# Kernel tuning notes

Measured on AMD Instinct MI355X. Metric: run time of the kernel, lower is better.

Reference implementation:

```python
import jax, jax.numpy as jnp
import numpy as np

N, E, G = 50000, 400000, 64
DIN, HID, H, ED = 128, 32, 8, 5
HC = H * HID            # 256, conv3 out_channels (concat=False, heads=1)
LH, DOUT = 256, 32
NEG_SLOPE = 0.2


def setup_inputs() -> dict:
    key = jax.random.key(0)
    ks = jax.random.split(key, 32)
    rn = lambda k, s, sc=0.05: (jax.random.normal(k, s, jnp.float32) * sc)
    inp = {
        "x": jax.random.normal(ks[0], (N, DIN), jnp.float32),
        "edge_index": jax.random.randint(ks[1], (2, E), 0, N, jnp.int32),
        "edge_attr": jax.random.uniform(ks[2], (E, ED), jnp.float32),
        "batch": jnp.sort(jax.random.randint(ks[3], (N,), 0, G, jnp.int32)),
        # conv1: in=DIN, heads=H, out=HID, concat=True
        "W1": rn(ks[4], (DIN, H * HID)), "as1": rn(ks[5], (H, HID)), "ad1": rn(ks[6], (H, HID)),
        "We1": rn(ks[7], (ED, H * HID)), "ae1": rn(ks[8], (H, HID)), "b1": jnp.zeros((H * HID,), jnp.float32),
        # conv2: in=H*HID, heads=H, out=HID, concat=True
        "W2": rn(ks[9], (H * HID, H * HID)), "as2": rn(ks[10], (H, HID)), "ad2": rn(ks[11], (H, HID)),
        "We2": rn(ks[12], (ED, H * HID)), "ae2": rn(ks[13], (H, HID)), "b2": jnp.zeros((H * HID,), jnp.float32),
        # conv3: in=H*HID, heads=1, out=HC, concat=False
        "W3": rn(ks[14], (H * HID, HC)), "as3": rn(ks[15], (1, HC)), "ad3": rn(ks[16], (1, HC)),
        "We3": rn(ks[17], (ED, HC)), "ae3": rn(ks[18], (1, HC)), "b3": jnp.zeros((HC,), jnp.float32),
        # MLP head
        "fcW1": rn(ks[19], (HC, LH)), "fcb1": jnp.zeros((LH,), jnp.float32),
        "fcW2": rn(ks[20], (LH, DOUT)), "fcb2": jnp.zeros((DOUT,), jnp.float32),
    }
    return inp


def gat_layer(x, src, dst, ea, W, att_s, att_d, We, att_e, bias, heads, out_ch, concat):
    n = x.shape[0]
    h = (x @ W).reshape(n, heads, out_ch)                 # [N,H,C]
    e = (ea @ We).reshape(-1, heads, out_ch)              # [E,H,C]
    a_s = (h * att_s).sum(-1)                             # [N,H]
    a_d = (h * att_d).sum(-1)                             # [N,H]
    a_e = (e * att_e).sum(-1)                             # [E,H]
    alpha = jax.nn.leaky_relu(a_s[src] + a_d[dst] + a_e, NEG_SLOPE)  # [E,H]
    m = jax.ops.segment_max(alpha, dst, num_segments=n)   # segment softmax over dst
    p = jnp.exp(alpha - m[dst])
    denom = jax.ops.segment_sum(p, dst, num_segments=n)
    w = p / (denom[dst] + 1e-16)                          # [E,H]
    msg = h[src] * w[:, :, None]                          # [E,H,C]
    out = jax.ops.segment_sum(msg, dst, num_segments=n)   # [N,H,C]
    out = out.reshape(n, heads * out_ch) if concat else out.mean(axis=1)
    return out + bias


def reference(x, edge_index, edge_attr, batch,
              W1, as1, ad1, We1, ae1, b1,
              W2, as2, ad2, We2, ae2, b2,
              W3, as3, ad3, We3, ae3, b3,
              fcW1, fcb1, fcW2, fcb2):
    src, dst = edge_index[0], edge_index[1]
    h = jax.nn.elu(gat_layer(x, src, dst, edge_attr, W1, as1, ad1, We1, ae1, b1, H, HID, True))
    h = jax.nn.elu(gat_layer(h, src, dst, edge_attr, W2, as2, ad2, We2, ae2, b2, H, HID, True))
    h = jax.nn.elu(gat_layer(h, src, dst, edge_attr, W3, as3, ad3, We3, ae3, b3, 1, HC, False))
    h = jax.nn.gelu(h @ fcW1 + fcb1, approximate=False) @ fcW2 + fcb2   # [N,DOUT]
    # global_mean_pool over batch ids
    sums = jax.ops.segment_sum(h, batch, num_segments=G)
    cnt = jax.ops.segment_sum(jnp.ones((h.shape[0],), h.dtype), batch, num_segments=G)
    return sums / jnp.maximum(cnt, 1.0)[:, None]
```

## Files before the change

### kernel.cpp

```cpp
#include <hip/hip_runtime.h>
#include <math.h>


#define N_NODES 50000
#define N_EDGES 400000
#define N_GRAPH 64
#define DIN     128
#define NHC     256
#define DOUT    32

typedef _Float16 f16x8 __attribute__((ext_vector_type(8)));
typedef _Float16 f16x4 __attribute__((ext_vector_type(4)));
typedef float    f32x4 __attribute__((ext_vector_type(4)));

#define LDP2 72

__device__ __forceinline__ void fma_mix_lo(float& acc, float pj, int w) {
    asm volatile("v_fma_mix_f32 %0, %1, %2, %0 op_sel:[0,0,0] op_sel_hi:[0,1,0]"
                 : "+v"(acc) : "v"(pj), "v"(w));
}
__device__ __forceinline__ void fma_mix_hi(float& acc, float pj, int w) {
    asm volatile("v_fma_mix_f32 %0, %1, %2, %0 op_sel:[0,1,0] op_sel_hi:[0,1,0]"
                 : "+v"(acc) : "v"(pj), "v"(w));
}

__global__ __launch_bounds__(256) void mfma_gemm_kernel(
    const _Float16* __restrict__ Ah, const _Float16* __restrict__ Bh,
    const float* __restrict__ bias, _Float16* __restrict__ Ch,
    const float* __restrict__ asl, const float* __restrict__ adl,
    float* __restrict__ asb, float* __restrict__ adb,
    const int* __restrict__ batch, float* __restrict__ pooled,
    int nrow, int K, int mode)
{
    __shared__ __align__(16) _Float16 sAh[128][LDP2];
    __shared__ __align__(16) _Float16 sBh[64][LDP2];

    const int tid = threadIdx.x, lane = tid & 63, wid = tid >> 6;
    const int wm = wid & 1, wn = wid >> 1;

    int xt, yt;
    if (gridDim.x == 4) {
        int bid = blockIdx.x + (blockIdx.y << 2);
        yt = (bid >> 5) * 8 + (bid & 7);
        xt = (bid >> 3) & 3;
    } else { xt = blockIdx.x; yt = blockIdx.y; }
    const int row0 = yt * 128, col0 = xt * 64;
    if (row0 >= nrow) return;

    const int frow = lane & 15, fk = (lane >> 4) * 8;

    f32x4 acc[4][2] = {};
    f16x8 pA[4], pB[2];

#pragma unroll
    for (int p = 0; p < 4; p++) {
        int idx = tid + p * 256;
        int r = idx >> 3, ch = (idx & 7) * 8;
        int gr = row0 + r;
        pA[p] = (gr < nrow) ? *(const f16x8*)(Ah + (long)gr * K + ch) : (f16x8)0;
    }
#pragma unroll
    for (int p = 0; p < 2; p++) {
        int idx = tid + p * 256;
        int r = idx >> 3, ch = (idx & 7) * 8;
        pB[p] = *(const f16x8*)(Bh + (long)(col0 + r) * K + ch);
    }

    for (int k0 = 0; k0 < K; k0 += 64) {
#pragma unroll
        for (int p = 0; p < 4; p++) {
            int idx = tid + p * 256;
            *(f16x8*)&sAh[idx >> 3][(idx & 7) * 8] = pA[p];
        }
#pragma unroll
        for (int p = 0; p < 2; p++) {
            int idx = tid + p * 256;
            *(f16x8*)&sBh[idx >> 3][(idx & 7) * 8] = pB[p];
        }
        __syncthreads();

        if (k0 + 64 < K) {
            int kn = k0 + 64;
#pragma unroll
            for (int p = 0; p < 4; p++) {
                int idx = tid + p * 256;
                int r = idx >> 3, ch = (idx & 7) * 8;
                int gr = row0 + r;
                pA[p] = (gr < nrow) ? *(const f16x8*)(Ah + (long)gr * K + kn + ch) : (f16x8)0;
            }
#pragma unroll
            for (int p = 0; p < 2; p++) {
                int idx = tid + p * 256;
                int r = idx >> 3, ch = (idx & 7) * 8;
                pB[p] = *(const f16x8*)(Bh + (long)(col0 + r) * K + kn + ch);
            }
        }

#pragma unroll
        for (int sub = 0; sub < 2; sub++) {
            const int fks = fk + sub * 32;
            f16x8 bh[2];
#pragma unroll
            for (int nt = 0; nt < 2; nt++)
                bh[nt] = *(const f16x8*)&sBh[wn * 32 + nt * 16 + frow][fks];
#pragma unroll
            for (int mt = 0; mt < 4; mt++) {
                f16x8 ah = *(const f16x8*)&sAh[wm * 64 + mt * 16 + frow][fks];
#pragma unroll
                for (int nt = 0; nt < 2; nt++)
                    acc[mt][nt] = __builtin_amdgcn_mfma_f32_16x16x32_f16(ah, bh[nt], acc[mt][nt], 0, 0, 0);
            }
        }
        __syncthreads();
    }

    const int crow0 = row0 + wm * 64 + (lane >> 4) * 4;
    const int ccol0 = col0 + wn * 32 + (lane & 15);

    if (mode == 0) {
#pragma unroll
        for (int mt = 0; mt < 4; mt++)
#pragma unroll
            for (int nt = 0; nt < 2; nt++) {
                int col = ccol0 + nt * 16;
#pragma unroll
                for (int r = 0; r < 4; r++) {
                    int row = crow0 + mt * 16 + r;
                    if (row < nrow) Ch[(long)row * 256 + col] = (_Float16)acc[mt][nt][r];
                }
            }
        if (asl != nullptr) {
            const float asl0 = asl[ccol0], asl1 = asl[ccol0 + 16];
            const float adl0 = adl[ccol0], adl1 = adl[ccol0 + 16];
            const int headw = (col0 + wn * 32) >> 5;
#pragma unroll
            for (int mt = 0; mt < 4; mt++) {
#pragma unroll
                for (int r = 0; r < 4; r++) {
                    float s = acc[mt][0][r] * asl0 + acc[mt][1][r] * asl1;
                    float d = acc[mt][0][r] * adl0 + acc[mt][1][r] * adl1;
                    s += __shfl_xor(s, 1); s += __shfl_xor(s, 2);
                    s += __shfl_xor(s, 4); s += __shfl_xor(s, 8);
                    d += __shfl_xor(d, 1); d += __shfl_xor(d, 2);
                    d += __shfl_xor(d, 4); d += __shfl_xor(d, 8);
                    if ((lane & 15) == 0) {
                        int row = crow0 + mt * 16 + r;
                        if (row < nrow) {
                            asb[row * 8 + headw] = s;
                            adb[row * 8 + headw] = d;
                        }
                    }
                }
            }
        }
    } else {
        float* pool = (float*)&sAh[0][0];
        const int g0 = batch[row0];
        const int rlast = (row0 + 127 < nrow) ? row0 + 127 : nrow - 1;
        const int gspan = batch[rlast] - g0 + 1;
        const bool fits = (gspan <= 16);
        for (int i = tid; i < 16 * 64; i += 256) pool[i] = 0.f;
        __syncthreads();

        const float b0 = bias[ccol0], b1 = bias[ccol0 + 16];
        const int lc0 = ccol0 - col0, lc1 = lc0 + 16;
        float sum0 = 0.f, sum1 = 0.f;
        int curg = -1;
#pragma unroll
        for (int mt = 0; mt < 4; mt++) {
#pragma unroll
            for (int r = 0; r < 4; r++) {
                int row = crow0 + mt * 16 + r;
                if (row >= nrow) continue;
                int g = batch[row];
                if (g != curg) {
                    if (curg >= 0) {
                        if (fits) {
                            atomicAdd(&pool[(curg - g0) * 64 + lc0], sum0);
                            atomicAdd(&pool[(curg - g0) * 64 + lc1], sum1);
                        } else {
                            atomicAdd(&pooled[curg * 256 + ccol0], sum0);
                            atomicAdd(&pooled[curg * 256 + ccol0 + 16], sum1);
                        }
                    }
                    curg = g; sum0 = 0.f; sum1 = 0.f;
                }
                float v0 = acc[mt][0][r] + b0;
                float v1 = acc[mt][1][r] + b1;
                sum0 += 0.5f * v0 * (1.f + erff(v0 * 0.7071067811865475f));
                sum1 += 0.5f * v1 * (1.f + erff(v1 * 0.7071067811865475f));
            }
        }
        if (curg >= 0) {
            if (fits) {
                atomicAdd(&pool[(curg - g0) * 64 + lc0], sum0);
                atomicAdd(&pool[(curg - g0) * 64 + lc1], sum1);
            } else {
                atomicAdd(&pooled[curg * 256 + ccol0], sum0);
                atomicAdd(&pooled[curg * 256 + ccol0 + 16], sum1);
            }
        }
        __syncthreads();
        if (fits) {
            for (int i = tid; i < gspan * 64; i += 256) {
                float val = pool[i];
                if (val != 0.f)
                    atomicAdd(&pooled[(g0 + (i >> 6)) * 256 + col0 + (i & 63)], val);
            }
        }
    }
}

#define J0 1600000
#define J1 32768
#define J2 65536
#define J3 65536
#define J4 65536
#define J5 16384
#define J6 N_NODES
#define J7 64
#define JTOT (J0+J1+J2+J3+J4+J5+J6+J7)

__device__ __forceinline__ void t_one(const float* W, _Float16* Bh,
                                      int id, int K, int realN)
{
    int n = id / K, k = id - n * K;
    Bh[id] = (_Float16)W[(long)k * realN + n];
}

__global__ __launch_bounds__(256) void prep_kernel(
    const float* __restrict__ x,
    const float* __restrict__ W1, const float* __restrict__ W2, const float* __restrict__ W3,
    const float* __restrict__ F1,
    _Float16* __restrict__ xh,
    _Float16* __restrict__ W1th, _Float16* __restrict__ W2th,
    _Float16* __restrict__ W3th, _Float16* __restrict__ F1th,
    float* __restrict__ pooled, int* __restrict__ deg, int* __restrict__ gcnt)
{
    int idx = blockIdx.x * 256 + threadIdx.x;
    if (idx < J0) {
        float4 v = ((const float4*)x)[idx];
        f16x4 h;
        h[0] = (_Float16)v.x; h[1] = (_Float16)v.y;
        h[2] = (_Float16)v.z; h[3] = (_Float16)v.w;
        *(f16x4*)(xh + (long)idx * 4) = h;
        return;
    }
    idx -= J0;
    if (idx < J1) { t_one(W1, W1th, idx, DIN, NHC); return; }
    idx -= J1;
    if (idx < J2) { t_one(W2, W2th, idx, NHC, NHC); return; }
    idx -= J2;
    if (idx < J3) { t_one(W3, W3th, idx, NHC, NHC); return; }
    idx -= J3;
    if (idx < J4) { t_one(F1, F1th, idx, NHC, NHC); return; }
    idx -= J4;
    if (idx < J5) { pooled[idx] = 0.f; return; }
    idx -= J5;
    if (idx < J6) { deg[idx] = 0; return; }
    idx -= J6;
    if (idx < J7) { gcnt[idx] = 0; return; }
}

__global__ void me_all_kernel(
    const float* __restrict__ We1, const float* __restrict__ ae1,
    const float* __restrict__ We2, const float* __restrict__ ae2,
    const float* __restrict__ We3, const float* __restrict__ ae3,
    float* __restrict__ MeAll)
{
    int l = blockIdx.x;
    const float* We = (l == 0) ? We1 : (l == 1) ? We2 : We3;
    const float* ae = (l == 0) ? ae1 : (l == 1) ? ae2 : ae3;
    int H = (l == 2) ? 1 : 8, C = (l == 2) ? 256 : 32;
    int t = threadIdx.x;
    if (t >= 5 * H) return;
    int j = t / H, hh = t - j * H;
    float s = 0.f;
    for (int c = 0; c < C; c++) s += We[j * NHC + hh * C + c] * ae[hh * C + c];
    MeAll[l * 40 + j * H + hh] = s;
}

__global__ __launch_bounds__(256) void asd_kernel(
    const _Float16* __restrict__ h, const float* __restrict__ atts, const float* __restrict__ attd,
    float* __restrict__ asb, float* __restrict__ adb, int total)
{
    int n = blockIdx.x * 256 + threadIdx.x;
    if (n >= total) return;
    const f16x8* hp = (const f16x8*)(h + (long)n * NHC);
    const float4* sp = (const float4*)atts;
    const float4* dp = (const float4*)attd;
    float ss = 0.f, dd = 0.f;
    for (int c = 0; c < NHC / 8; c++) {
        f16x8 hv = hp[c];
        float4 s1 = sp[2 * c], s2 = sp[2 * c + 1];
        float4 d1 = dp[2 * c], d2 = dp[2 * c + 1];
        ss += (float)hv[0] * s1.x + (float)hv[1] * s1.y + (float)hv[2] * s1.z + (float)hv[3] * s1.w
            + (float)hv[4] * s2.x + (float)hv[5] * s2.y + (float)hv[6] * s2.z + (float)hv[7] * s2.w;
        dd += (float)hv[0] * d1.x + (float)hv[1] * d1.y + (float)hv[2] * d1.z + (float)hv[3] * d1.w
            + (float)hv[4] * d2.x + (float)hv[5] * d2.y + (float)hv[6] * d2.z + (float)hv[7] * d2.w;
    }
    asb[n * 8] = ss; adb[n * 8] = dd;
}

__global__ __launch_bounds__(256) void count_hist_kernel(
    const int* __restrict__ ei, const int* __restrict__ batch,
    int* __restrict__ deg, int* __restrict__ gcnt, int E, int N)
{
    __shared__ int hist[N_GRAPH];
    int t = threadIdx.x;
    if (t < N_GRAPH) hist[t] = 0;
    __syncthreads();
    int i = blockIdx.x * 256 + t;
    if (i < E) atomicAdd(&deg[ei[E + i]], 1);
    if (i < N) atomicAdd(&hist[batch[i]], 1);
    __syncthreads();
    if (t < N_GRAPH && hist[t] > 0) atomicAdd(&gcnt[t], hist[t]);
}

__global__ __launch_bounds__(256) void scan_block_kernel(
    const int* __restrict__ deg, int* __restrict__ rowstart, int* __restrict__ partial, int n)
{
    __shared__ int s[256];
    int i = blockIdx.x * 256 + threadIdx.x;
    int v = (i < n) ? deg[i] : 0;
    s[threadIdx.x] = v;
    __syncthreads();
    for (int off = 1; off < 256; off <<= 1) {
        int t = (threadIdx.x >= off) ? s[threadIdx.x - off] : 0;
        __syncthreads();
        s[threadIdx.x] += t;
        __syncthreads();
    }
    if (i < n) rowstart[i] = s[threadIdx.x] - v;
    if (threadIdx.x == 255) partial[blockIdx.x] = s[255];
}

__global__ __launch_bounds__(256) void scan_partial_kernel(int* __restrict__ partial, int nb)
{
    __shared__ int s[256];
    int v = (threadIdx.x < nb) ? partial[threadIdx.x] : 0;
    s[threadIdx.x] = v;
    __syncthreads();
    for (int off = 1; off < 256; off <<= 1) {
        int t = (threadIdx.x >= off) ? s[threadIdx.x - off] : 0;
        __syncthreads();
        s[threadIdx.x] += t;
        __syncthreads();
    }
    if (threadIdx.x < nb) partial[threadIdx.x] = s[threadIdx.x] - v;
}

__global__ __launch_bounds__(256) void scan_add_kernel(
    int* __restrict__ rowstart, const int* __restrict__ partial, int* __restrict__ cursor,
    int n, int E)
{
    int i = blockIdx.x * 256 + threadIdx.x;
    if (i < n) {
        int v = rowstart[i] + partial[blockIdx.x];
        rowstart[i] = v;
        cursor[i] = v;
    }
    if (i == 0) rowstart[n] = E;
}

__global__ __launch_bounds__(256) void fill_kernel(
    const int* __restrict__ ei, int* __restrict__ cursor, int2* __restrict__ csr2, int E)
{
    int e = blockIdx.x * 256 + threadIdx.x;
    if (e >= E) return;
    int dst = ei[E + e];
    int pos = atomicAdd(&cursor[dst], 1);
    csr2[pos] = make_int2(ei[e], e);
}

__global__ __launch_bounds__(256) void aec_kernel(
    const int2* __restrict__ csr2, const float* __restrict__ ea,
    const float* __restrict__ MeAll,
    int* __restrict__ csr, _Float16* __restrict__ aec, int E)
{
    int pos = blockIdx.x * 256 + threadIdx.x;
    if (pos >= E) return;
    int2 se = csr2[pos];
    csr[pos] = se.x;
    const float* eap = ea + (long)se.y * 5;
    float e0 = eap[0], e1 = eap[1], e2 = eap[2], e3 = eap[3], e4 = eap[4];
#pragma unroll
    for (int l = 0; l < 2; l++) {
        const float* Me = MeAll + l * 40;
        f16x8 v;
#pragma unroll
        for (int hh = 0; hh < 8; hh++) {
            float s = e0 * Me[hh] + e1 * Me[8 + hh] + e2 * Me[16 + hh]
                    + e3 * Me[24 + hh] + e4 * Me[32 + hh];
            v[hh] = (_Float16)s;
        }
        *(f16x8*)(aec + (long)l * N_EDGES * 8 + (long)pos * 8) = v;
    }
    const float* Me2 = MeAll + 80;
    float s2 = e0 * Me2[0] + e1 * Me2[1] + e2 * Me2[2] + e3 * Me2[3] + e4 * Me2[4];
    f16x8 v2;
#pragma unroll
    for (int hh = 0; hh < 8; hh++) v2[hh] = (_Float16)s2;
    *(f16x8*)(aec + (long)2 * N_EDGES * 8 + (long)pos * 8) = v2;
}

__global__ __launch_bounds__(256) void gat_agg_kernel(
    const int* __restrict__ rowstart, const int* __restrict__ csr,
    const _Float16* __restrict__ aec, const float* __restrict__ asb,
    const float* __restrict__ adb,
    const _Float16* __restrict__ h, const float* __restrict__ bias,
    _Float16* __restrict__ Oh, int H, int clog2)
{
    int node = blockIdx.x * 4 + (threadIdx.x >> 6);
    if (node >= N_NODES) return;
    const int lane = threadIdx.x & 63;
    const int half = lane >> 5;
    const int c8   = (lane & 31) * 8;
    const int hc   = c8 >> clog2;
    const int heff = lane & (H - 1);
    const int grp  = lane >> 3;

    const float adn = adb[node * 8 + heff];
    const int beg = rowstart[node], end = rowstart[node + 1];

    float acc[8] = {};
    float den = 0.f;

    for (int i = beg; i < end; i += 8) {
        int idx = i + grp;
        const bool valid = (idx < end);
        if (!valid) idx = end - 1;
        const int sj = csr[idx];
        const float ae = (float)aec[(long)idx * 8 + heff];
        float al = asb[sj * 8 + heff] + adn + ae;
        al = fmaxf(al, 0.2f * al);
        const float pv = valid ? __expf(al) : 0.f;
#pragma unroll
        for (int jj = 0; jj < 4; jj++) {
            const int j = jj * 2 + half;
            const float pj = __shfl(pv, j * 8 + hc);
            const int srcj = __shfl(sj, j * 8);
            const int4 hw = *(const int4*)(h + (long)srcj * NHC + c8);
            den += pj;
            fma_mix_lo(acc[0], pj, hw.x); fma_mix_hi(acc[1], pj, hw.x);
            fma_mix_lo(acc[2], pj, hw.y); fma_mix_hi(acc[3], pj, hw.y);
            fma_mix_lo(acc[4], pj, hw.z); fma_mix_hi(acc[5], pj, hw.z);
            fma_mix_lo(acc[6], pj, hw.w); fma_mix_hi(acc[7], pj, hw.w);
        }
    }

    den += __shfl_xor(den, 32);
#pragma unroll
    for (int k = 0; k < 8; k++)
        acc[k] += __shfl_xor(acc[k], 32);

    if (half == 0) {
        const float w = 1.0f / (den + 1e-16f);
        const float4 b0 = *(const float4*)(bias + c8);
        const float4 b1 = *(const float4*)(bias + c8 + 4);
        const float bb[8] = {b0.x, b0.y, b0.z, b0.w, b1.x, b1.y, b1.z, b1.w};
        f16x8 oh;
#pragma unroll
        for (int k = 0; k < 8; k++) {
            float v = acc[k] * w + bb[k];
            v = (v > 0.f) ? v : (__expf(v) - 1.f);
            oh[k] = (_Float16)v;
        }
        *(f16x8*)(Oh + (long)node * NHC + c8) = oh;
    }
}

__global__ void final_kernel(const float* __restrict__ pooled, const int* __restrict__ gcnt,
                             const float* __restrict__ fcW2, const float* __restrict__ fcb2,
                             float* __restrict__ out)
{
    int g = blockIdx.x;
    int j = threadIdx.x;
    if (j >= DOUT) return;
    float s = 0.f;
    for (int k = 0; k < NHC; k++) s += pooled[g * NHC + k] * fcW2[k * DOUT + j];
    int c = gcnt[g];
    out[g * DOUT + j] = (c > 0) ? (s / (float)c + fcb2[j]) : 0.f;
}

extern "C" void kernel_launch(void* const* d_in, const int* in_sizes, int n_in,
                              void* d_out, int out_size, void* d_ws, size_t ws_size,
                              hipStream_t stream)
{
    const float* x    = (const float*)d_in[0];
    const int*   ei   = (const int*)  d_in[1];
    const float* ea   = (const float*)d_in[2];
    const int*   bat  = (const int*)  d_in[3];
    const float* W[3]   = {(const float*)d_in[4],  (const float*)d_in[10], (const float*)d_in[16]};
    const float* Asl[3] = {(const float*)d_in[5],  (const float*)d_in[11], (const float*)d_in[17]};
    const float* Adl[3] = {(const float*)d_in[6],  (const float*)d_in[12], (const float*)d_in[18]};
    const float* Wel[3] = {(const float*)d_in[7],  (const float*)d_in[13], (const float*)d_in[19]};
    const float* Ael[3] = {(const float*)d_in[8],  (const float*)d_in[14], (const float*)d_in[20]};
    const float* Bil[3] = {(const float*)d_in[9],  (const float*)d_in[15], (const float*)d_in[21]};
    const float* fcW1 = (const float*)d_in[22];
    const float* fcb1 = (const float*)d_in[23];
    const float* fcW2 = (const float*)d_in[24];
    const float* fcb2 = (const float*)d_in[25];

    char* w = (char*)d_ws;
    _Float16* h    = (_Float16*)w;     w += (size_t)N_NODES * NHC * 2;
    _Float16* xh   = (_Float16*)w;     w += (size_t)N_NODES * DIN * 2;
    _Float16* xbh  = (_Float16*)w;     w += (size_t)N_NODES * NHC * 2;
    float*    asb  = (float*)w;        w += (size_t)N_NODES * 8 * 4;
    float*    adb  = (float*)w;        w += (size_t)N_NODES * 8 * 4;
    float*    MeAll= (float*)w;        w += 120 * 4;
    float*    pooled=(float*)w;        w += (size_t)N_GRAPH * NHC * 4;
    _Float16* W1th = (_Float16*)w;     w += (size_t)NHC * DIN * 2;
    _Float16* W2th = (_Float16*)w;     w += (size_t)NHC * NHC * 2;
    _Float16* W3th = (_Float16*)w;     w += (size_t)NHC * NHC * 2;
    _Float16* F1th = (_Float16*)w;     w += (size_t)NHC * NHC * 2;
    int* gcnt     = (int*)w;           w += N_GRAPH * 4;
    int* deg      = (int*)w;           w += (size_t)N_NODES * 4;
    int* rowstart = (int*)w;           w += (size_t)(N_NODES + 1) * 4;
    int* cursor   = (int*)w;           w += (size_t)N_NODES * 4;
    int* partial  = (int*)w;           w += 256 * 4;
    w = (char*)(((size_t)w + 15) & ~(size_t)15);
    int2* csr2    = (int2*)w;          w += (size_t)N_EDGES * 8;
    int* csr      = (int*)w;           w += (size_t)N_EDGES * 4;
    w = (char*)(((size_t)w + 15) & ~(size_t)15);
    _Float16* aec = (_Float16*)w;      w += (size_t)3 * N_EDGES * 8 * 2;

    const int NB = (N_NODES + 255) / 256;

    prep_kernel<<<(JTOT + 255) / 256, 256, 0, stream>>>(
        x, W[0], W[1], W[2], fcW1,
        xh, W1th, W2th, W3th, F1th,
        pooled, deg, gcnt);
    count_hist_kernel<<<(N_EDGES + 255) / 256, 256, 0, stream>>>(ei, bat, deg, gcnt, N_EDGES, N_NODES);
    scan_block_kernel<<<NB, 256, 0, stream>>>(deg, rowstart, partial, N_NODES);
    scan_partial_kernel<<<1, 256, 0, stream>>>(partial, NB);
    scan_add_kernel<<<NB, 256, 0, stream>>>(rowstart, partial, cursor, N_NODES, N_EDGES);
    me_all_kernel<<<3, 64, 0, stream>>>(Wel[0], Ael[0], Wel[1], Ael[1], Wel[2], Ael[2], MeAll);
    fill_kernel<<<(N_EDGES + 255) / 256, 256, 0, stream>>>(ei, cursor, csr2, N_EDGES);
    aec_kernel<<<(N_EDGES + 255) / 256, 256, 0, stream>>>(csr2, ea, MeAll, csr, aec, N_EDGES);

    const int Hs[3] = {8, 8, 1};
    const int CL[3] = {5, 5, 8};
    const int Ks[3] = {DIN, NHC, NHC};

    const dim3 ggrid(4, 392);

    const _Float16* curh = xh;
    const _Float16* Wth[3] = {W1th, W2th, W3th};
    for (int l = 0; l < 3; l++) {
        const int H = Hs[l];
        const bool fuse = (l != 2);
        mfma_gemm_kernel<<<ggrid, 256, 0, stream>>>(
            curh, Wth[l], nullptr, h,
            fuse ? Asl[l] : nullptr, fuse ? Adl[l] : nullptr, asb, adb,
            nullptr, nullptr,
            N_NODES, Ks[l], 0);
        if (!fuse)
            asd_kernel<<<(N_NODES + 255) / 256, 256, 0, stream>>>(
                h, Asl[l], Adl[l], asb, adb, N_NODES);
        gat_agg_kernel<<<(N_NODES + 3) / 4, 256, 0, stream>>>(
            rowstart, csr, aec + (size_t)l * N_EDGES * 8, asb, adb, h, Bil[l], xbh, H, CL[l]);
        curh = xbh;
    }

    mfma_gemm_kernel<<<ggrid, 256, 0, stream>>>(
        xbh, F1th, fcb1, nullptr,
        nullptr, nullptr, nullptr, nullptr,
        bat, pooled,
        N_NODES, NHC, 3);
    final_kernel<<<N_GRAPH, 64, 0, stream>>>(pooled, gcnt, fcW2, fcb2, (float*)d_out);
}
```

Baseline: 435.8 us.

## Widen GEMM block tile to 128x128 with K-step 32 and one-wave columns

The MFMA GEMM block tile grows from 128x64 to 128x128. Each of the four waves now owns a 32-column strip across all 128 rows, and the K step shrinks from 64 to 32 with smaller padded LDS rows. The grid is halved in x and the swizzle and pooling epilogue are adjusted to match. This raises reuse of the A operand and cuts redundant A loads across column tiles, at the cost of more accumulator registers per thread, more barriers per K, and fewer blocks in flight.

```diff
diff --git a/kernel.cpp b/kernel.cpp
--- a/kernel.cpp
+++ b/kernel.cpp
@@ -13,7 +13,7 @@
 typedef _Float16 f16x4 __attribute__((ext_vector_type(4)));
 typedef float    f32x4 __attribute__((ext_vector_type(4)));
 
-#define LDP2 72
+#define LDP3 40
 
 __device__ __forceinline__ void fma_mix_lo(float& acc, float pj, int w) {
     asm volatile("v_fma_mix_f32 %0, %1, %2, %0 op_sel:[0,0,0] op_sel_hi:[0,1,0]"
@@ -32,94 +32,74 @@
     const int* __restrict__ batch, float* __restrict__ pooled,
     int nrow, int K, int mode)
 {
-    __shared__ __align__(16) _Float16 sAh[128][LDP2];
-    __shared__ __align__(16) _Float16 sBh[64][LDP2];
-
-    const int tid = threadIdx.x, lane = tid & 63, wid = tid >> 6;
-    const int wm = wid & 1, wn = wid >> 1;
+    __shared__ __align__(16) _Float16 sAh[128][LDP3];
+    __shared__ __align__(16) _Float16 sBh[128][LDP3];
+
+    const int tid = threadIdx.x, lane = tid & 63, wn = tid >> 6;
 
     int xt, yt;
-    if (gridDim.x == 4) {
-        int bid = blockIdx.x + (blockIdx.y << 2);
-        yt = (bid >> 5) * 8 + (bid & 7);
-        xt = (bid >> 3) & 3;
+    if (gridDim.x == 2) {
+        int bid = blockIdx.x + (blockIdx.y << 1);
+        yt = (bid >> 4) * 8 + (bid & 7);
+        xt = (bid >> 3) & 1;
     } else { xt = blockIdx.x; yt = blockIdx.y; }
-    const int row0 = yt * 128, col0 = xt * 64;
+    const int row0 = yt * 128, col0 = xt * 128;
     if (row0 >= nrow) return;
 
     const int frow = lane & 15, fk = (lane >> 4) * 8;
-
-    f32x4 acc[4][2] = {};
-    f16x8 pA[4], pB[2];
-
-#pragma unroll
-    for (int p = 0; p < 4; p++) {
-        int idx = tid + p * 256;
-        int r = idx >> 3, ch = (idx & 7) * 8;
+    const int sr = tid >> 2, sch = (tid & 3) * 8;
+
+    f32x4 acc[8][2] = {};
+    f16x8 pA[2], pB[2];
+
+#pragma unroll
+    for (int p = 0; p < 2; p++) {
+        int r = sr + p * 64;
         int gr = row0 + r;
-        pA[p] = (gr < nrow) ? *(const f16x8*)(Ah + (long)gr * K + ch) : (f16x8)0;
-    }
-#pragma unroll
-    for (int p = 0; p < 2; p++) {
-        int idx = tid + p * 256;
-        int r = idx >> 3, ch = (idx & 7) * 8;
-        pB[p] = *(const f16x8*)(Bh + (long)(col0 + r) * K + ch);
-    }
-
-    for (int k0 = 0; k0 < K; k0 += 64) {
-#pragma unroll
-        for (int p = 0; p < 4; p++) {
-            int idx = tid + p * 256;
-            *(f16x8*)&sAh[idx >> 3][(idx & 7) * 8] = pA[p];
-        }
+        pA[p] = (gr < nrow) ? *(const f16x8*)(Ah + (long)gr * K + sch) : (f16x8)0;
+        pB[p] = *(const f16x8*)(Bh + (long)(col0 + r) * K + sch);
+    }
+
+    for (int k0 = 0; k0 < K; k0 += 32) {
 #pragma unroll
         for (int p = 0; p < 2; p++) {
-            int idx = tid + p * 256;
-            *(f16x8*)&sBh[idx >> 3][(idx & 7) * 8] = pB[p];
-        }
-        __syncthreads();
-
-        if (k0 + 64 < K) {
-            int kn = k0 + 64;
-#pragma unroll
-            for (int p = 0; p < 4; p++) {
-                int idx = tid + p * 256;
-                int r = idx >> 3, ch = (idx & 7) * 8;
+            int r = sr + p * 64;
+            *(f16x8*)&sAh[r][sch] = pA[p];
+            *(f16x8*)&sBh[r][sch] = pB[p];
+        }
+        __syncthreads();
+
+        if (k0 + 32 < K) {
+            int kn = k0 + 32;
+#pragma unroll
+            for (int p = 0; p < 2; p++) {
+                int r = sr + p * 64;
                 int gr = row0 + r;
-                pA[p] = (gr < nrow) ? *(const f16x8*)(Ah + (long)gr * K + kn + ch) : (f16x8)0;
+                pA[p] = (gr < nrow) ? *(const f16x8*)(Ah + (long)gr * K + kn + sch) : (f16x8)0;
+                pB[p] = *(const f16x8*)(Bh + (long)(col0 + r) * K + kn + sch);
             }
-#pragma unroll
-            for (int p = 0; p < 2; p++) {
-                int idx = tid + p * 256;
-                int r = idx >> 3, ch = (idx & 7) * 8;
-                pB[p] = *(const f16x8*)(Bh + (long)(col0 + r) * K + kn + ch);
-            }
-        }
-
-#pragma unroll
-        for (int sub = 0; sub < 2; sub++) {
-            const int fks = fk + sub * 32;
-            f16x8 bh[2];
+        }
+
+        f16x8 bh[2];
+#pragma unroll
+        for (int nt = 0; nt < 2; nt++)
+            bh[nt] = *(const f16x8*)&sBh[wn * 32 + nt * 16 + frow][fk];
+#pragma unroll
+        for (int mt = 0; mt < 8; mt++) {
+            f16x8 ah = *(const f16x8*)&sAh[mt * 16 + frow][fk];
 #pragma unroll
             for (int nt = 0; nt < 2; nt++)
-                bh[nt] = *(const f16x8*)&sBh[wn * 32 + nt * 16 + frow][fks];
-#pragma unroll
-            for (int mt = 0; mt < 4; mt++) {
-                f16x8 ah = *(const f16x8*)&sAh[wm * 64 + mt * 16 + frow][fks];
-#pragma unroll
-                for (int nt = 0; nt < 2; nt++)
-                    acc[mt][nt] = __builtin_amdgcn_mfma_f32_16x16x32_f16(ah, bh[nt], acc[mt][nt], 0, 0, 0);
-            }
-        }
-        __syncthreads();
-    }
-
-    const int crow0 = row0 + wm * 64 + (lane >> 4) * 4;
+                acc[mt][nt] = __builtin_amdgcn_mfma_f32_16x16x32_f16(ah, bh[nt], acc[mt][nt], 0, 0, 0);
+        }
+        __syncthreads();
+    }
+
+    const int crow0 = row0 + (lane >> 4) * 4;
     const int ccol0 = col0 + wn * 32 + (lane & 15);
 
     if (mode == 0) {
 #pragma unroll
-        for (int mt = 0; mt < 4; mt++)
+        for (int mt = 0; mt < 8; mt++)
 #pragma unroll
             for (int nt = 0; nt < 2; nt++) {
                 int col = ccol0 + nt * 16;
@@ -132,9 +112,9 @@
         if (asl != nullptr) {
             const float asl0 = asl[ccol0], asl1 = asl[ccol0 + 16];
             const float adl0 = adl[ccol0], adl1 = adl[ccol0 + 16];
-            const int headw = (col0 + wn * 32) >> 5;
-#pragma unroll
-            for (int mt = 0; mt < 4; mt++) {
+            const int headw = (col0 >> 5) + wn;
+#pragma unroll
+            for (int mt = 0; mt < 8; mt++) {
 #pragma unroll
                 for (int r = 0; r < 4; r++) {
                     float s = acc[mt][0][r] * asl0 + acc[mt][1][r] * asl1;
@@ -159,7 +139,7 @@
         const int rlast = (row0 + 127 < nrow) ? row0 + 127 : nrow - 1;
         const int gspan = batch[rlast] - g0 + 1;
         const bool fits = (gspan <= 16);
-        for (int i = tid; i < 16 * 64; i += 256) pool[i] = 0.f;
+        for (int i = tid; i < 16 * 128; i += 256) pool[i] = 0.f;
         __syncthreads();
 
         const float b0 = bias[ccol0], b1 = bias[ccol0 + 16];
@@ -167,7 +147,7 @@
         float sum0 = 0.f, sum1 = 0.f;
         int curg = -1;
 #pragma unroll
-        for (int mt = 0; mt < 4; mt++) {
+        for (int mt = 0; mt < 8; mt++) {
 #pragma unroll
             for (int r = 0; r < 4; r++) {
                 int row = crow0 + mt * 16 + r;
@@ -176,8 +156,8 @@
                 if (g != curg) {
                     if (curg >= 0) {
                         if (fits) {
-                            atomicAdd(&pool[(curg - g0) * 64 + lc0], sum0);
-                            atomicAdd(&pool[(curg - g0) * 64 + lc1], sum1);
+                            atomicAdd(&pool[(curg - g0) * 128 + lc0], sum0);
+                            atomicAdd(&pool[(curg - g0) * 128 + lc1], sum1);
                         } else {
                             atomicAdd(&pooled[curg * 256 + ccol0], sum0);
                             atomicAdd(&pooled[curg * 256 + ccol0 + 16], sum1);
@@ -193,8 +173,8 @@
         }
         if (curg >= 0) {
             if (fits) {
-                atomicAdd(&pool[(curg - g0) * 64 + lc0], sum0);
-                atomicAdd(&pool[(curg - g0) * 64 + lc1], sum1);
+                atomicAdd(&pool[(curg - g0) * 128 + lc0], sum0);
+                atomicAdd(&pool[(curg - g0) * 128 + lc1], sum1);
             } else {
                 atomicAdd(&pooled[curg * 256 + ccol0], sum0);
                 atomicAdd(&pooled[curg * 256 + ccol0 + 16], sum1);
@@ -202,10 +182,10 @@
         }
         __syncthreads();
         if (fits) {
-            for (int i = tid; i < gspan * 64; i += 256) {
+            for (int i = tid; i < gspan * 128; i += 256) {
                 float val = pool[i];
                 if (val != 0.f)
-                    atomicAdd(&pooled[(g0 + (i >> 6)) * 256 + col0 + (i & 63)], val);
+                    atomicAdd(&pooled[(g0 + (i >> 7)) * 256 + col0 + (i & 127)], val);
             }
         }
     }
@@ -543,7 +523,7 @@
     const int CL[3] = {5, 5, 8};
     const int Ks[3] = {DIN, NHC, NHC};
 
-    const dim3 ggrid(4, 392);
+    const dim3 ggrid(2, 392);
 
     const _Float16* curh = xh;
     const _Float16* Wth[3] = {W1th, W2th, W3th};
```

Result: slower. 453.6 us (+4.1%).
